# Performance work log

Measured on AMD Instinct MI355X. Metric: run time of the kernel, lower is better.

The kernel has to match this reference:

```python
import jax, jax.numpy as jnp
import numpy as np

NEG_SLOPE = 0.2


def setup_inputs() -> dict:
    key = jax.random.key(0)
    ks = jax.random.split(key, 12)
    Nm, Na, E, Din, H, D = 50000, 50000, 400000, 128, 8, 32
    return {
        "master_feats": jax.random.normal(ks[0], (Nm, Din), jnp.float32),
        "attn_feats0": jax.random.normal(ks[1], (Na, Din), jnp.float32),
        "attn_feats1": jax.random.normal(ks[2], (Na, Din), jnp.float32),
        "src0": jax.random.randint(ks[3], (E,), 0, Na, jnp.int32),
        "dst0": jax.random.randint(ks[4], (E,), 0, Nm, jnp.int32),
        "src1": jax.random.randint(ks[5], (E,), 0, Na, jnp.int32),
        "dst1": jax.random.randint(ks[6], (E,), 0, Nm, jnp.int32),
        "W_master": jax.random.normal(ks[7], (Din, H * D), jnp.float32) * 0.08,
        "W0": jax.random.normal(ks[8], (Din, H * D), jnp.float32) * 0.08,
        "W1": jax.random.normal(ks[9], (Din, H * D), jnp.float32) * 0.08,
        "attn_l": jax.random.normal(ks[10], (H, D), jnp.float32) * 0.1,
        "attn_r": jax.random.normal(ks[11], (H, D), jnp.float32) * 0.1,
    }


def reference(master_feats, attn_feats0, attn_feats1, src0, dst0, src1, dst1,
              W_master, W0, W1, attn_l, attn_r):
    Nm = master_feats.shape[0]
    H, D = attn_l.shape

    # Per-node-type linear projections (no bias) + attention logits.
    ft_m = (master_feats @ W_master).reshape(Nm, H, D)        # [Nm,H,D]
    er = jnp.einsum("nhd,hd->nh", ft_m, attn_r)               # [Nm,H]

    def proj(feats, W):
        ft = (feats @ W).reshape(feats.shape[0], H, D)
        el = jnp.einsum("nhd,hd->nh", ft, attn_l)
        return ft, el

    ft0, el0 = proj(attn_feats0, W0)
    ft1, el1 = proj(attn_feats1, W1)

    lrelu = lambda x: jnp.where(x >= 0, x, NEG_SLOPE * x)
    e0 = lrelu(el0[src0] + er[dst0])                          # [E0,H]
    e1 = lrelu(el1[src1] + er[dst1])                          # [E1,H]

    # Heterograph edge softmax: normalize over ALL incoming edges of each
    # master node, regardless of source node type (subtract dst-max for
    # stability; mathematically identical to the conditional path in source).
    dst = jnp.concatenate([dst0, dst1])
    e = jnp.concatenate([e0, e1], axis=0)                     # [E0+E1,H]
    emax = jax.ops.segment_max(e, dst, num_segments=Nm)
    emax = jnp.where(jnp.isfinite(emax), emax, 0.0)           # nodes w/o edges
    ee = jnp.exp(e - emax[dst])
    esum = jax.ops.segment_sum(ee, dst, num_segments=Nm)
    a = ee / esum[dst]                                        # [E0+E1,H]

    # u_mul_e + sum aggregation onto master nodes.
    E0 = src0.shape[0]
    msg = jnp.concatenate(
        [ft0[src0] * a[:E0, :, None], ft1[src1] * a[E0:, :, None]], axis=0
    )                                                         # [E,H,D]
    rst = jax.ops.segment_sum(msg, dst, num_segments=Nm)      # [Nm,H,D]
    return rst
```

## Files before the change

kernel.cpp:

```cpp
#include <hip/hip_runtime.h>
#include <cstdint>
#include <cstddef>

#define NEG_SLOPE 0.2f

typedef __attribute__((ext_vector_type(8))) short short8;
typedef __attribute__((ext_vector_type(4))) float f32x4;

static __device__ __forceinline__ unsigned short f2bf(float x) {
  uint32_t u = __float_as_uint(x);
  uint32_t r = (u + 0x7FFFu + ((u >> 16) & 1u)) >> 16;
  return (unsigned short)r;
}
static __device__ __forceinline__ float bf2f(unsigned short b) {
  return __uint_as_float(((uint32_t)b) << 16);
}

__global__ void wt_kernel(const float* __restrict__ W0, const float* __restrict__ W1,
                          const float* __restrict__ W2,
                          unsigned short* __restrict__ T0, unsigned short* __restrict__ T1,
                          unsigned short* __restrict__ T2) {
  const float* W = (blockIdx.y == 0) ? W0 : (blockIdx.y == 1) ? W1 : W2;
  unsigned short* T = (blockIdx.y == 0) ? T0 : (blockIdx.y == 1) ? T1 : T2;
  int c = blockIdx.x * 2 + (threadIdx.x >> 7);
  int k = threadIdx.x & 127;
  T[c * 128 + k] = f2bf(W[k * 256 + c]);
}

__global__ __launch_bounds__(256)
void proj_mfma_kernel(const float* __restrict__ fm, const float* __restrict__ fa0,
                      const float* __restrict__ fa1,
                      const unsigned short* __restrict__ Wtm,
                      const unsigned short* __restrict__ Wt0,
                      const unsigned short* __restrict__ Wt1,
                      const float* __restrict__ attn_l, const float* __restrict__ attn_r,
                      int Nm, int Na0, int Na1,
                      unsigned short* __restrict__ ft_all, float* __restrict__ el_all,
                      float* __restrict__ er) {
  const int z = blockIdx.z;
  const float* feats = (z == 0) ? fm : (z == 1) ? fa0 : fa1;
  const unsigned short* Wt = (z == 0) ? Wtm : (z == 1) ? Wt0 : Wt1;
  const float* av = (z == 0) ? attn_r : attn_l;
  const int N = (z == 0) ? Nm : (z == 1) ? Na0 : Na1;
  unsigned short* ft_out = (z == 0) ? nullptr
                         : (z == 1) ? ft_all : ft_all + (size_t)Na0 * 256;
  float* el_out = (z == 0) ? er : (z == 1) ? el_all : el_all + (size_t)Na0 * 8;

  const int rb = blockIdx.x * 128;
  if (rb >= N) return;

  const int t = threadIdx.x;
  const int wid = t >> 6, lane = t & 63;
  const int wm = wid >> 1, wn = wid & 1;
  const int l15 = lane & 15, l4 = lane >> 4;

  const int arow = rb + wm * 64 + l15;
  short8 af[4][4];
  #pragma unroll
  for (int mf = 0; mf < 4; ++mf) {
    int row = arow + mf * 16;
    const float* rp = &feats[(size_t)row * 128];
    bool ok = row < N;
    #pragma unroll
    for (int kb = 0; kb < 4; ++kb) {
      float4 lo = make_float4(0.f, 0.f, 0.f, 0.f), hi = lo;
      if (ok) {
        lo = *(const float4*)(rp + kb * 32 + l4 * 8);
        hi = *(const float4*)(rp + kb * 32 + l4 * 8 + 4);
      }
      short8 v;
      v[0] = f2bf(lo.x); v[1] = f2bf(lo.y); v[2] = f2bf(lo.z); v[3] = f2bf(lo.w);
      v[4] = f2bf(hi.x); v[5] = f2bf(hi.y); v[6] = f2bf(hi.z); v[7] = f2bf(hi.w);
      af[kb][mf] = v;
    }
  }

  #pragma unroll
  for (int cbi = 0; cbi < 2; ++cbi) {
    const int cbw = cbi * 128 + wn * 64;
    const int head0 = cbw >> 5;

    short8 bf[4][4];
    #pragma unroll
    for (int nf = 0; nf < 4; ++nf) {
      const unsigned short* wp = &Wt[(size_t)(cbw + nf * 16 + l15) * 128];
      #pragma unroll
      for (int kb = 0; kb < 4; ++kb)
        bf[kb][nf] = *(const short8*)(wp + kb * 32 + l4 * 8);
    }

    f32x4 acc[4][4];
    #pragma unroll
    for (int a = 0; a < 4; ++a)
      #pragma unroll
      for (int b = 0; b < 4; ++b)
        acc[a][b] = (f32x4){0.f, 0.f, 0.f, 0.f};

    #pragma unroll
    for (int kb = 0; kb < 4; ++kb)
      #pragma unroll
      for (int mf = 0; mf < 4; ++mf)
        #pragma unroll
        for (int nf = 0; nf < 4; ++nf)
          acc[mf][nf] = __builtin_amdgcn_mfma_f32_16x16x32_bf16(
              bf[kb][nf], af[kb][mf], acc[mf][nf], 0, 0, 0);

    float avf[4][4];
    #pragma unroll
    for (int nf = 0; nf < 4; ++nf)
      #pragma unroll
      for (int reg = 0; reg < 4; ++reg)
        avf[nf][reg] = av[(head0 + (nf >> 1)) * 32 + (nf & 1) * 16 + l4 * 4 + reg];

    #pragma unroll
    for (int mf = 0; mf < 4; ++mf) {
      int node = arow + mf * 16;
      bool ok = node < N;
      if (ft_out != nullptr && ok) {
        size_t base = (size_t)node * 256 + cbw + l4 * 4;
        #pragma unroll
        for (int nf = 0; nf < 4; ++nf) {
          ushort4 u;
          u.x = f2bf(acc[mf][nf][0]); u.y = f2bf(acc[mf][nf][1]);
          u.z = f2bf(acc[mf][nf][2]); u.w = f2bf(acc[mf][nf][3]);
          *(ushort4*)(&ft_out[base + nf * 16]) = u;
        }
      }
      #pragma unroll
      for (int hh = 0; hh < 2; ++hh) {
        float p = 0.f;
        #pragma unroll
        for (int reg = 0; reg < 4; ++reg) {
          p = fmaf(acc[mf][2 * hh][reg], avf[2 * hh][reg], p);
          p = fmaf(acc[mf][2 * hh + 1][reg], avf[2 * hh + 1][reg], p);
        }
        p += __shfl_xor(p, 16);
        p += __shfl_xor(p, 32);
        if (ok && l4 == 0)
          el_out[(size_t)node * 8 + head0 + hh] = p;
      }
    }
  }
}

__global__ void count_deg_kernel(const int* __restrict__ dst0, int E0,
                                 const int* __restrict__ dst1, int E1,
                                 int* __restrict__ deg) {
  int E = E0 + E1;
  for (int i = blockIdx.x * blockDim.x + threadIdx.x; i < E;
       i += gridDim.x * blockDim.x) {
    int d = (i < E0) ? dst0[i] : dst1[i - E0];
    atomicAdd(&deg[d], 1);
  }
}

__global__ __launch_bounds__(1024)
void block_reduce_kernel(const int* __restrict__ deg, int* __restrict__ partial, int n) {
  __shared__ int wsum[16];
  const int t = threadIdx.x;
  int idx = blockIdx.x * 1024 + t;
  int v = (idx < n) ? deg[idx] : 0;
  #pragma unroll
  for (int off = 1; off < 64; off <<= 1) v += __shfl_xor(v, off);
  if ((t & 63) == 0) wsum[t >> 6] = v;
  __syncthreads();
  if (t < 16) {
    int x = wsum[t];
    #pragma unroll
    for (int off = 1; off < 16; off <<= 1) x += __shfl_xor(x, off);
    if (t == 0) partial[blockIdx.x] = x;
  }
}

__global__ __launch_bounds__(64)
void partial_scan_kernel(const int* __restrict__ partial, int* __restrict__ base,
                         int nb, int* __restrict__ offs, int n) {
  const int t = threadIdx.x;
  int v = (t < nb) ? partial[t] : 0;
  int incl = v;
  #pragma unroll
  for (int off = 1; off < 64; off <<= 1) {
    int x = __shfl_up(incl, off);
    if (t >= off) incl += x;
  }
  if (t < nb) base[t] = incl - v;
  if (t == nb - 1) offs[n] = incl;
}

__global__ __launch_bounds__(1024)
void apply_scan_kernel(const int* __restrict__ deg, const int* __restrict__ base,
                       int* __restrict__ offs, int* __restrict__ cursor, int n) {
  __shared__ int wsum[16];
  const int t = threadIdx.x;
  const int idx = blockIdx.x * 1024 + t;
  int v = (idx < n) ? deg[idx] : 0;
  const int lane = t & 63, w = t >> 6;
  int incl = v;
  #pragma unroll
  for (int off = 1; off < 64; off <<= 1) {
    int x = __shfl_up(incl, off);
    if (lane >= off) incl += x;
  }
  if (lane == 63) wsum[w] = incl;
  __syncthreads();
  if (t < 16) {
    int x = wsum[t];
    #pragma unroll
    for (int off = 1; off < 16; off <<= 1) {
      int y = __shfl_up(x, off);
      if (t >= off) x += y;
    }
    wsum[t] = x;
  }
  __syncthreads();
  int excl = base[blockIdx.x] + ((w > 0) ? wsum[w - 1] : 0) + incl - v;
  if (idx < n) {
    offs[idx] = excl;
    cursor[idx] = excl;
  }
}

__global__ void scatter_kernel(const int* __restrict__ src0, const int* __restrict__ dst0, int E0,
                               const int* __restrict__ src1, const int* __restrict__ dst1, int E1,
                               int* __restrict__ cursor, int* __restrict__ slots,
                               uint4* __restrict__ wslots,
                               const float* __restrict__ el, const float* __restrict__ er,
                               int Na0) {
  int E = E0 + E1;
  for (int i = blockIdx.x * blockDim.x + threadIdx.x; i < E;
       i += gridDim.x * blockDim.x) {
    int s, d;
    if (i < E0) { s = src0[i]; d = dst0[i]; }
    else        { s = src1[i - E0] + Na0; d = dst1[i - E0]; }
    int pos = atomicAdd(&cursor[d], 1);
    slots[pos] = s;

    const float* elp = &el[(size_t)s * 8];
    const float* erp = &er[(size_t)d * 8];
    float4 ea = *(const float4*)elp, eb = *(const float4*)(elp + 4);
    float4 ra = *(const float4*)erp, rb = *(const float4*)(erp + 4);
    float w[8];
    w[0] = ea.x + ra.x; w[1] = ea.y + ra.y; w[2] = ea.z + ra.z; w[3] = ea.w + ra.w;
    w[4] = eb.x + rb.x; w[5] = eb.y + rb.y; w[6] = eb.z + rb.z; w[7] = eb.w + rb.w;
    uint4 pk;
    uint32_t* pku = (uint32_t*)&pk;
    #pragma unroll
    for (int q = 0; q < 4; ++q) {
      float v0 = w[2 * q], v1 = w[2 * q + 1];
      v0 = fmaxf(v0, NEG_SLOPE * v0);
      v1 = fmaxf(v1, NEG_SLOPE * v1);
      uint32_t b0 = f2bf(__expf(v0)), b1 = f2bf(__expf(v1));
      pku[q] = b0 | (b1 << 16);
    }
    wslots[pos] = pk;
  }
}

__global__ __launch_bounds__(256)
void aggregate_kernel(const int* __restrict__ offs, const int* __restrict__ slots,
                      const unsigned short* __restrict__ wsl,
                      const unsigned short* __restrict__ ft,
                      float* __restrict__ rst, int Nm) {
  int gid = blockIdx.x * blockDim.x + threadIdx.x;
  int n = gid >> 6;
  int lane = threadIdx.x & 63;
  if (n >= Nm) return;
  int beg = offs[n], end = offs[n + 1];
  int h = lane >> 3;
  float o0 = 0.f, o1 = 0.f, o2 = 0.f, o3 = 0.f;
  if (beg < end) {
    float sw = 0.f;
    float w0 = 0.f, w1 = 0.f, w2 = 0.f, w3 = 0.f, w4 = 0.f, w5 = 0.f, w6 = 0.f, w7 = 0.f;
    ushort4 f0 = {0,0,0,0}, f1 = f0, f2 = f0, f3 = f0, f4 = f0, f5 = f0, f6 = f0, f7 = f0;

#define LD(idx, ww, ff)                                                          \
    do {                                                                         \
      if ((idx) < end) {                                                         \
        ww = bf2f(wsl[(size_t)(uint32_t)(idx) * 8 + h]);                         \
        int s_ = slots[(idx)];                                                   \
        ff = *(const ushort4*)((const char*)ft +                                 \
                               (((size_t)(uint32_t)s_) << 9) + lane * 8);        \
      }                                                                          \
    } while (0)

#define PR(ww, ff)                                                               \
    do {                                                                         \
      sw += ww;                                                                  \
      o0 = fmaf(ww, bf2f(ff.x), o0);                                             \
      o1 = fmaf(ww, bf2f(ff.y), o1);                                             \
      o2 = fmaf(ww, bf2f(ff.z), o2);                                             \
      o3 = fmaf(ww, bf2f(ff.w), o3);                                             \
    } while (0)

    LD(beg + 0, w0, f0); LD(beg + 1, w1, f1); LD(beg + 2, w2, f2); LD(beg + 3, w3, f3);
    LD(beg + 4, w4, f4); LD(beg + 5, w5, f5); LD(beg + 6, w6, f6); LD(beg + 7, w7, f7);

    for (int i = beg; i < end; i += 8) {
      PR(w0, f0); LD(i + 8, w0, f0);
      if (i + 1 < end) { PR(w1, f1); LD(i + 9,  w1, f1); }
      if (i + 2 < end) { PR(w2, f2); LD(i + 10, w2, f2); }
      if (i + 3 < end) { PR(w3, f3); LD(i + 11, w3, f3); }
      if (i + 4 < end) { PR(w4, f4); LD(i + 12, w4, f4); }
      if (i + 5 < end) { PR(w5, f5); LD(i + 13, w5, f5); }
      if (i + 6 < end) { PR(w6, f6); LD(i + 14, w6, f6); }
      if (i + 7 < end) { PR(w7, f7); LD(i + 15, w7, f7); }
    }
#undef LD
#undef PR
    float inv = 1.0f / sw;
    o0 *= inv; o1 *= inv; o2 *= inv; o3 *= inv;
  }
  *(float4*)(&rst[(size_t)n * 256 + lane * 4]) = make_float4(o0, o1, o2, o3);
}

extern "C" void kernel_launch(void* const* d_in, const int* in_sizes, int n_in,
                              void* d_out, int out_size, void* d_ws, size_t ws_size,
                              hipStream_t stream) {
  const float* master = (const float*)d_in[0];
  const float* af0    = (const float*)d_in[1];
  const float* af1    = (const float*)d_in[2];
  const int*   src0   = (const int*)d_in[3];
  const int*   dst0   = (const int*)d_in[4];
  const int*   src1   = (const int*)d_in[5];
  const int*   dst1   = (const int*)d_in[6];
  const float* Wm     = (const float*)d_in[7];
  const float* W0     = (const float*)d_in[8];
  const float* W1     = (const float*)d_in[9];
  const float* attn_l = (const float*)d_in[10];
  const float* attn_r = (const float*)d_in[11];

  const int Nm  = in_sizes[0] / 128;
  const int Na0 = in_sizes[1] / 128;
  const int Na1 = in_sizes[2] / 128;
  const int E0  = in_sizes[3];
  const int E1  = in_sizes[5];
  float* rst = (float*)d_out;

  char* ws = (char*)d_ws;
  size_t off = 0;
  auto alloc = [&](size_t b) -> char* {
    char* p = ws + off;
    off += (b + 511) & ~(size_t)511;
    return p;
  };
  unsigned short* ft = (unsigned short*)alloc((size_t)(Na0 + Na1) * 256 * sizeof(unsigned short));
  float* el = (float*)alloc((size_t)(Na0 + Na1) * 8 * sizeof(float));
  float* er = (float*)alloc((size_t)Nm * 8 * sizeof(float));
  unsigned short* Wtm = (unsigned short*)alloc(256 * 128 * sizeof(unsigned short));
  unsigned short* Wt0 = (unsigned short*)alloc(256 * 128 * sizeof(unsigned short));
  unsigned short* Wt1 = (unsigned short*)alloc(256 * 128 * sizeof(unsigned short));
  int* deg     = (int*)alloc((size_t)Nm * sizeof(int));
  int* offs    = (int*)alloc((size_t)(Nm + 1) * sizeof(int));
  int* cursor  = (int*)alloc((size_t)Nm * sizeof(int));
  int* partial = (int*)alloc(64 * sizeof(int));
  int* pbase   = (int*)alloc(64 * sizeof(int));
  int* slots   = (int*)alloc((size_t)(E0 + E1) * sizeof(int));
  uint4* wslots = (uint4*)alloc((size_t)(E0 + E1) * sizeof(uint4));

  wt_kernel<<<dim3(128, 3), 256, 0, stream>>>(Wm, W0, W1, Wtm, Wt0, Wt1);

  int Nmax = Nm > Na0 ? Nm : Na0; if (Na1 > Nmax) Nmax = Na1;
  const int mb = (Nmax + 127) / 128;
  proj_mfma_kernel<<<dim3(mb, 1, 3), 256, 0, stream>>>(
      master, af0, af1, Wtm, Wt0, Wt1, attn_l, attn_r,
      Nm, Na0, Na1, ft, el, er);

  hipMemsetAsync(deg, 0, (size_t)Nm * sizeof(int), stream);
  count_deg_kernel<<<1024, 256, 0, stream>>>(dst0, E0, dst1, E1, deg);
  const int nb = (Nm + 1023) / 1024;
  block_reduce_kernel<<<nb, 1024, 0, stream>>>(deg, partial, Nm);
  partial_scan_kernel<<<1, 64, 0, stream>>>(partial, pbase, nb, offs, Nm);
  apply_scan_kernel<<<nb, 1024, 0, stream>>>(deg, pbase, offs, cursor, Nm);
  scatter_kernel<<<1024, 256, 0, stream>>>(src0, dst0, E0, src1, dst1, E1,
                                           cursor, slots, wslots, el, er, Na0);

  aggregate_kernel<<<(Nm + 3) / 4, 256, 0, stream>>>(offs, slots,
                                                     (const unsigned short*)wslots,
                                                     ft, rst, Nm);
}
```

Before: 241.8 us.

## Stage projection A tile in swizzled LDS and pack edge src+weights into records

The projection kernel now loads the feature tile once with coalesced float4 reads, converts it to bf16 into an XOR-swizzled shared-memory buffer, and reads MFMA A fragments from LDS per k-block, which cuts register pressure and improves global coalescing. Separately, the scatter kernel writes a 32-byte record per edge holding the source index and the eight bf16 weights, replacing the separate slots and weight arrays. The aggregate kernel then reads both from one cache line per edge instead of two scattered loads. The cost is a 32 KB LDS allocation and a barrier in the projection, and twice the edge-record bytes written, since 12 of each 32 bytes are padding.

Result: faster. 230.8 us (-4.6%).

```diff
diff --git a/kernel.cpp b/kernel.cpp
--- a/kernel.cpp
+++ b/kernel.cpp
@@ -49,31 +49,26 @@
   const int rb = blockIdx.x * 128;
   if (rb >= N) return;
 
+  __shared__ unsigned short As[128 * 128 / 2 * 2];
   const int t = threadIdx.x;
+
+  #pragma unroll
+  for (int it = 0; it < 16; ++it) {
+    int i = it * 256 + t;
+    int r = i >> 5, kc = (i & 31) << 2;
+    float4 f = make_float4(0.f, 0.f, 0.f, 0.f);
+    if (rb + r < N) f = *(const float4*)(&feats[(size_t)(rb + r) * 128 + kc]);
+    ushort4 u;
+    u.x = f2bf(f.x); u.y = f2bf(f.y); u.z = f2bf(f.z); u.w = f2bf(f.w);
+    uint32_t byte = ((uint32_t)(r * 256 + kc * 2)) ^ ((uint32_t)((r & 7) << 4));
+    *(ushort4*)((char*)As + byte) = u;
+  }
+  __syncthreads();
+
   const int wid = t >> 6, lane = t & 63;
   const int wm = wid >> 1, wn = wid & 1;
   const int l15 = lane & 15, l4 = lane >> 4;
-
   const int arow = rb + wm * 64 + l15;
-  short8 af[4][4];
-  #pragma unroll
-  for (int mf = 0; mf < 4; ++mf) {
-    int row = arow + mf * 16;
-    const float* rp = &feats[(size_t)row * 128];
-    bool ok = row < N;
-    #pragma unroll
-    for (int kb = 0; kb < 4; ++kb) {
-      float4 lo = make_float4(0.f, 0.f, 0.f, 0.f), hi = lo;
-      if (ok) {
-        lo = *(const float4*)(rp + kb * 32 + l4 * 8);
-        hi = *(const float4*)(rp + kb * 32 + l4 * 8 + 4);
-      }
-      short8 v;
-      v[0] = f2bf(lo.x); v[1] = f2bf(lo.y); v[2] = f2bf(lo.z); v[3] = f2bf(lo.w);
-      v[4] = f2bf(hi.x); v[5] = f2bf(hi.y); v[6] = f2bf(hi.z); v[7] = f2bf(hi.w);
-      af[kb][mf] = v;
-    }
-  }
 
   #pragma unroll
   for (int cbi = 0; cbi < 2; ++cbi) {
@@ -97,13 +92,21 @@
         acc[a][b] = (f32x4){0.f, 0.f, 0.f, 0.f};
 
     #pragma unroll
-    for (int kb = 0; kb < 4; ++kb)
+    for (int kb = 0; kb < 4; ++kb) {
+      short8 af[4];
+      #pragma unroll
+      for (int mf = 0; mf < 4; ++mf) {
+        int row = wm * 64 + mf * 16 + l15;
+        uint32_t byte = ((uint32_t)(row * 256 + kb * 64 + l4 * 16)) ^ ((uint32_t)((row & 7) << 4));
+        af[mf] = *(const short8*)((const char*)As + byte);
+      }
       #pragma unroll
       for (int mf = 0; mf < 4; ++mf)
         #pragma unroll
         for (int nf = 0; nf < 4; ++nf)
           acc[mf][nf] = __builtin_amdgcn_mfma_f32_16x16x32_bf16(
-              bf[kb][nf], af[kb][mf], acc[mf][nf], 0, 0, 0);
+              bf[kb][nf], af[mf], acc[mf][nf], 0, 0, 0);
+    }
 
     float avf[4][4];
     #pragma unroll
@@ -222,8 +225,7 @@
 
 __global__ void scatter_kernel(const int* __restrict__ src0, const int* __restrict__ dst0, int E0,
                                const int* __restrict__ src1, const int* __restrict__ dst1, int E1,
-                               int* __restrict__ cursor, int* __restrict__ slots,
-                               uint4* __restrict__ wslots,
+                               int* __restrict__ cursor, char* __restrict__ recs,
                                const float* __restrict__ el, const float* __restrict__ er,
                                int Na0) {
   int E = E0 + E1;
@@ -233,7 +235,6 @@
     if (i < E0) { s = src0[i]; d = dst0[i]; }
     else        { s = src1[i - E0] + Na0; d = dst1[i - E0]; }
     int pos = atomicAdd(&cursor[d], 1);
-    slots[pos] = s;
 
     const float* elp = &el[(size_t)s * 8];
     const float* erp = &er[(size_t)d * 8];
@@ -242,23 +243,23 @@
     float w[8];
     w[0] = ea.x + ra.x; w[1] = ea.y + ra.y; w[2] = ea.z + ra.z; w[3] = ea.w + ra.w;
     w[4] = eb.x + rb.x; w[5] = eb.y + rb.y; w[6] = eb.z + rb.z; w[7] = eb.w + rb.w;
-    uint4 pk;
-    uint32_t* pku = (uint32_t*)&pk;
+    uint32_t pk[4];
     #pragma unroll
     for (int q = 0; q < 4; ++q) {
       float v0 = w[2 * q], v1 = w[2 * q + 1];
       v0 = fmaxf(v0, NEG_SLOPE * v0);
       v1 = fmaxf(v1, NEG_SLOPE * v1);
       uint32_t b0 = f2bf(__expf(v0)), b1 = f2bf(__expf(v1));
-      pku[q] = b0 | (b1 << 16);
-    }
-    wslots[pos] = pk;
+      pk[q] = b0 | (b1 << 16);
+    }
+    char* rp = recs + ((size_t)(uint32_t)pos << 5);
+    *(uint4*)rp = make_uint4((uint32_t)s, pk[0], pk[1], pk[2]);
+    *(uint4*)(rp + 16) = make_uint4(pk[3], 0u, 0u, 0u);
   }
 }
 
 __global__ __launch_bounds__(256)
-void aggregate_kernel(const int* __restrict__ offs, const int* __restrict__ slots,
-                      const unsigned short* __restrict__ wsl,
+void aggregate_kernel(const int* __restrict__ offs, const char* __restrict__ recs,
                       const unsigned short* __restrict__ ft,
                       float* __restrict__ rst, int Nm) {
   int gid = blockIdx.x * blockDim.x + threadIdx.x;
@@ -267,6 +268,7 @@
   if (n >= Nm) return;
   int beg = offs[n], end = offs[n + 1];
   int h = lane >> 3;
+  const int hoff = 4 + ((h >> 1) << 2);
   float o0 = 0.f, o1 = 0.f, o2 = 0.f, o3 = 0.f;
   if (beg < end) {
     float sw = 0.f;
@@ -276,8 +278,10 @@
 #define LD(idx, ww, ff)                                                          \
     do {                                                                         \
       if ((idx) < end) {                                                         \
-        ww = bf2f(wsl[(size_t)(uint32_t)(idx) * 8 + h]);                         \
-        int s_ = slots[(idx)];                                                   \
+        const char* rp_ = recs + ((size_t)(uint32_t)(idx) << 5);                 \
+        int s_ = *(const int*)rp_;                                               \
+        uint32_t wv_ = *(const uint32_t*)(rp_ + hoff);                           \
+        ww = __uint_as_float((h & 1) ? (wv_ & 0xffff0000u) : (wv_ << 16));       \
         ff = *(const ushort4*)((const char*)ft +                                 \
                                (((size_t)(uint32_t)s_) << 9) + lane * 8);        \
       }                                                                          \
@@ -354,8 +358,7 @@
   int* cursor  = (int*)alloc((size_t)Nm * sizeof(int));
   int* partial = (int*)alloc(64 * sizeof(int));
   int* pbase   = (int*)alloc(64 * sizeof(int));
-  int* slots   = (int*)alloc((size_t)(E0 + E1) * sizeof(int));
-  uint4* wslots = (uint4*)alloc((size_t)(E0 + E1) * sizeof(uint4));
+  char* recs   = alloc((size_t)(E0 + E1) * 32);
 
   wt_kernel<<<dim3(128, 3), 256, 0, stream>>>(Wm, W0, W1, Wtm, Wt0, Wt1);
 
@@ -372,9 +375,7 @@
   partial_scan_kernel<<<1, 64, 0, stream>>>(partial, pbase, nb, offs, Nm);
   apply_scan_kernel<<<nb, 1024, 0, stream>>>(deg, pbase, offs, cursor, Nm);
   scatter_kernel<<<1024, 256, 0, stream>>>(src0, dst0, E0, src1, dst1, E1,
-                                           cursor, slots, wslots, el, er, Na0);
-
-  aggregate_kernel<<<(Nm + 3) / 4, 256, 0, stream>>>(offs, slots,
-                                                     (const unsigned short*)wslots,
-                                                     ft, rst, Nm);
-}
+                                           cursor, recs, el, er, Na0);
+
+  aggregate_kernel<<<(Nm + 3) / 4, 256, 0, stream>>>(offs, recs, ft, rst, Nm);
+}
```
